# Kernel optimization log

Measured on AMD Instinct MI355X. Metric: run time of the kernel, lower is better.

Reference implementation:

```python
import jax, jax.numpy as jnp
import numpy as np

K_MASK = -2.3819763e+38

B, T, D = 2, 2048, 2048
N_HEADS, N_KV, HEAD_DIM = 16, 8, 128
SCALAR = 0.08838834764831845  # head_dim ** -0.5
ROPE_BASE = 10000


def rms_norm(x, scale):
    # fp32 mean-of-squares, rsqrt, bf16 round-trip, then scale (as in QwemmaRMSNorm)
    x32 = x.astype(jnp.float32)
    var = jnp.mean(jnp.square(x32), axis=-1, keepdims=True)
    rescaled = (x32 * jax.lax.rsqrt(var + 1e-06)).astype(jnp.bfloat16)
    return rescaled * scale


def apply_rope(inputs, positions, base_frequency):
    head_dim = inputs.shape[-1]
    fraction = 2 * jnp.arange(0, head_dim // 2) / head_dim
    timescale = base_frequency ** fraction
    sinusoid = positions[..., jnp.newaxis] / timescale[jnp.newaxis, jnp.newaxis, :]
    sinusoid = sinusoid[..., jnp.newaxis, :]  # [B,T,1,H/2]
    sin = jnp.sin(sinusoid).astype(inputs.dtype)
    cos = jnp.cos(sinusoid).astype(inputs.dtype)
    first, second = jnp.split(inputs, 2, axis=-1)
    out = jnp.concatenate([first * cos - second * sin,
                           second * cos + first * sin], axis=-1)
    return out.astype(inputs.dtype)


def setup_inputs() -> dict:
    key = jax.random.key(0)
    ks = jax.random.split(key, 7)
    x = jax.random.normal(ks[0], (B, T, D), dtype=jnp.float32)
    segment_pos = jnp.broadcast_to(jnp.arange(T, dtype=jnp.int32)[None, :], (B, T))
    attn_mask = jnp.broadcast_to(jnp.tril(jnp.ones((T, T), dtype=bool))[None], (B, T, T))
    q_w = jax.random.normal(ks[1], (N_HEADS, D, HEAD_DIM), dtype=jnp.float32) * 0.02
    kv_w = jax.random.normal(ks[2], (2, N_KV, D, HEAD_DIM), dtype=jnp.float32) * 0.02
    o_w = jax.random.normal(ks[3], (N_HEADS, HEAD_DIM, D), dtype=jnp.float32) * 0.02
    q_scale = 1.0 + 0.1 * jax.random.normal(ks[4], (HEAD_DIM,), dtype=jnp.float32)
    k_scale = 1.0 + 0.1 * jax.random.normal(ks[5], (HEAD_DIM,), dtype=jnp.float32)
    return {"x": x, "segment_pos": segment_pos, "attn_mask": attn_mask,
            "q_w": q_w, "kv_w": kv_w, "o_w": o_w,
            "q_scale": q_scale, "k_scale": k_scale}


def reference(x, segment_pos, attn_mask, q_w, kv_w, o_w, q_scale, k_scale):
    # projections
    q = jnp.einsum('BTD,NDH->BTNH', x, q_w)
    k, v = jnp.einsum('BSD,CKDH->CBSKH', x, kv_w)
    # QK RMSNorm + RoPE
    q = apply_rope(rms_norm(q, q_scale), segment_pos, ROPE_BASE)
    k = apply_rope(rms_norm(k, k_scale), segment_pos, ROPE_BASE)
    # GQA: [B,T,N,H] -> [B,T,K,G,H]
    b, t, n, h = q.shape
    g = n // N_KV
    q = q.reshape((b, t, N_KV, g, h))
    logits = jnp.einsum('BTKGH,BSKH->BTKGS', q, k)
    logits = (logits.astype(jnp.float32) * SCALAR).astype(jnp.bfloat16)
    s = logits.shape[-1]
    logits = logits.reshape((b, t, n, s))
    padded = jnp.where(jnp.expand_dims(attn_mask, -2), logits, K_MASK)
    probs = jax.nn.softmax(padded.astype(jnp.float32), axis=-1).astype(k.dtype)
    probs = probs.reshape((b, t, N_KV, g, s))
    encoded = jnp.einsum('BTKGS,BSKH->BTKGH', probs, v)
    encoded = encoded.reshape((b, t, n, h))
    return jnp.einsum('BTNH,NHD->BTD', encoded, o_w)


if __name__ == '__main__':
    out = reference(**setup_inputs())
    print(out.shape, out.dtype)
```

## Files before the change

### kernel.cpp

```cpp
#include <hip/hip_runtime.h>

typedef unsigned short u16;
typedef __attribute__((ext_vector_type(4))) float f32x4;
typedef __attribute__((ext_vector_type(8))) short s16x8;

#define SCALAR_F 0.08838834764831845f
#define KMASKF (-1e30f)

__device__ __forceinline__ u16 f2b(float f){
  unsigned u = __float_as_uint(f);
  unsigned r = u + 0x7FFFu + ((u>>16)&1u);
  return (u16)(r>>16);
}
__device__ __forceinline__ float b2f(u16 h){ return __uint_as_float(((unsigned)h)<<16); }

__device__ __forceinline__ f32x4 mfma16(s16x8 a, s16x8 b, f32x4 c){
  return __builtin_amdgcn_mfma_f32_16x16x32_bf16(a, b, c, 0, 0, 0);
}

__device__ __forceinline__ void glds16(const u16* g, u16* l){
  __builtin_amdgcn_global_load_lds((const __attribute__((address_space(1))) unsigned*)g,
                                   (__attribute__((address_space(3))) unsigned*)l, 16, 0, 0);
}

__global__ __launch_bounds__(256) void cvt_f32_bf16(const float* __restrict__ in, u16* __restrict__ out){
  int i = blockIdx.x*256 + threadIdx.x;
  const float4* p = (const float4*)in;
  float4 a = p[2*i], b = p[2*i+1];
  s16x8 r;
  r[0]=(short)f2b(a.x); r[1]=(short)f2b(a.y); r[2]=(short)f2b(a.z); r[3]=(short)f2b(a.w);
  r[4]=(short)f2b(b.x); r[5]=(short)f2b(b.y); r[6]=(short)f2b(b.z); r[7]=(short)f2b(b.w);
  *(s16x8*)(out + (size_t)i*8) = r;
}

__global__ __launch_bounds__(256) void build_wqkvt(const float* __restrict__ qw, const float* __restrict__ kvw,
                                                   u16* __restrict__ out){
  __shared__ float t[64][65];
  int head = blockIdx.z;
  int d0 = blockIdx.y*64, h0 = blockIdx.x*64;
  const float* src; int colbase;
  if (head < 16){ src = qw + (size_t)head*2048*128; colbase = head*128; }
  else if (head < 24){ int k = head-16; src = kvw + (size_t)k*2048*128; colbase = 2048 + k*128; }
  else { int k = head-24; src = kvw + (size_t)(8+k)*2048*128; colbase = 3072 + k*128; }
  int tid = threadIdx.x;
  #pragma unroll
  for (int p=0;p<16;p++){ int e = p*256+tid; int r = e>>6, c = e&63;
    t[r][c] = src[(size_t)(d0+r)*128 + h0 + c]; }
  __syncthreads();
  #pragma unroll
  for (int p=0;p<16;p++){ int e = p*256+tid; int c = e>>6, r = e&63;
    out[(size_t)(colbase + h0 + c)*2048 + d0 + r] = f2b(t[r][c]); }
}

__global__ __launch_bounds__(256) void tr2048(const float* __restrict__ src, u16* __restrict__ out){
  __shared__ float t[64][65];
  int r0 = blockIdx.y*64, c0 = blockIdx.x*64;
  int tid = threadIdx.x;
  #pragma unroll
  for (int p=0;p<16;p++){ int e = p*256+tid; int r = e>>6, c = e&63;
    t[r][c] = src[(size_t)(r0+r)*2048 + c0 + c]; }
  __syncthreads();
  #pragma unroll
  for (int p=0;p<16;p++){ int e = p*256+tid; int c = e>>6, r = e&63;
    out[(size_t)(c0+c)*2048 + r0 + r] = f2b(t[r][c]); }
}

__global__ __launch_bounds__(256) void rope_table(float* __restrict__ table){
  int tid = blockIdx.x*256 + threadIdx.x;
  int pos = tid>>6, i = tid&63;
  float ts = powf(10000.f, (float)i * (1.f/64.f));
  float ang = (float)pos / ts;
  ((float2*)table)[tid] = make_float2(sinf(ang), cosf(ang));
}

__global__ __launch_bounds__(512,2) void gemm256(const u16* __restrict__ A, const u16* __restrict__ Bt,
                                                 u16* __restrict__ C, int K, int ldc){
  __shared__ u16 Asw[4][256*32];
  __shared__ u16 Bsw[4][256*32];
  const int tid = threadIdx.x;
  const int wid = tid>>6, l = tid&63;
  const int wr = wid>>2, wc = wid&3;
  const int l15 = l&15, lg = l>>4;
  const int wg = blockIdx.x;
  const int swz = (wg&7)*32 + (wg>>3);
  const size_t m0 = (size_t)(swz>>4)*256, n0 = (size_t)(swz&15)*256;

  const f32x4 z4 = {0.f,0.f,0.f,0.f};
  f32x4 acc[8][4];
  #pragma unroll
  for (int mi=0;mi<8;mi++)
    #pragma unroll
    for (int ni=0;ni<4;ni++) acc[mi][ni] = z4;

  auto stage = [&](int k0, int bi){
    #pragma unroll
    for (int c=0;c<2;c++){
      int g = c*512 + tid;
      int row = g>>2;
      int sc = (g&3) ^ ((g>>3)&3);
      glds16(A  + (m0+row)*K + k0 + sc*8, &Asw[bi][0] + g*8);
      glds16(Bt + (n0+row)*K + k0 + sc*8, &Bsw[bi][0] + g*8);
    }
  };

  auto compute = [&](int bi){
    const char* AsB = (const char*)&Asw[bi][0];
    const char* BsB = (const char*)&Bsw[bi][0];
    s16x8 bfr[4];
    #pragma unroll
    for (int ni=0;ni<4;ni++){
      int r = wc*64 + ni*16 + l15;
      bfr[ni] = *(const s16x8*)(BsB + r*64 + ((lg*16) ^ (((r>>1)&3)<<4)));
    }
    __builtin_amdgcn_s_setprio(1);
    #pragma unroll
    for (int mi=0;mi<8;mi++){
      int r = wr*128 + mi*16 + l15;
      s16x8 af = *(const s16x8*)(AsB + r*64 + ((lg*16) ^ (((r>>1)&3)<<4)));
      #pragma unroll
      for (int ni=0;ni<4;ni++)
        acc[mi][ni] = mfma16(af, bfr[ni], acc[mi][ni]);
    }
    __builtin_amdgcn_s_setprio(0);
  };

  const int NT = K>>5;
  stage(0,0); stage(32,1); stage(64,2);
  asm volatile("s_waitcnt vmcnt(8)" ::: "memory");
  __builtin_amdgcn_s_barrier();
  for (int t=0; t<NT; ++t){
    if (t+3 < NT) stage((t+3)<<5, (t+3)&3);
    compute(t&3);
    int rem = NT-1-t;
    if (rem >= 3)      { asm volatile("s_waitcnt vmcnt(8)" ::: "memory"); }
    else if (rem == 2) { asm volatile("s_waitcnt vmcnt(4)" ::: "memory"); }
    else if (rem == 1) { asm volatile("s_waitcnt vmcnt(0)" ::: "memory"); }
    __builtin_amdgcn_s_barrier();
  }

  #pragma unroll
  for (int mi=0;mi<8;mi++)
    #pragma unroll
    for (int ni=0;ni<4;ni++)
      #pragma unroll
      for (int r=0;r<4;r++){
        size_t row = m0 + wr*128 + mi*16 + lg*4 + r;
        size_t col = n0 + wc*64 + ni*16 + l15;
        C[row*ldc + col] = f2b(acc[mi][ni][r]);
      }
}

template<bool OUTBF16>
__global__ __launch_bounds__(256) void gemm_bt(const u16* __restrict__ A, const u16* __restrict__ Bt,
                                               void* __restrict__ C, int K, int ldc){
  __shared__ u16 As[128*64];
  __shared__ u16 Bs[128*64];
  const int tid = threadIdx.x, w = tid>>6, l = tid&63;
  const int wm = w>>1, wn = w&1;
  const int l15 = l&15, lg = l>>4, l7 = l&7;
  const size_t m0 = (size_t)blockIdx.y*128, n0 = (size_t)blockIdx.x*128;
  const f32x4 z4 = {0.f,0.f,0.f,0.f};
  f32x4 acc[4][4];
  #pragma unroll
  for (int m=0;m<4;m++)
    #pragma unroll
    for (int n=0;n<4;n++) acc[m][n] = z4;
  const char* AsB = (const char*)As; const char* BsB = (const char*)Bs;
  int colsw[2];
  colsw[0] = (lg*16) ^ (l7<<4);
  colsw[1] = (64 + lg*16) ^ (l7<<4);
  int arow[4], brow[4];
  #pragma unroll
  for (int m=0;m<4;m++){ arow[m] = (wm*64 + m*16 + l15)*128; brow[m] = (wn*64 + m*16 + l15)*128; }
  const int sgl = l7 ^ (l>>3);
  for (int k0=0;k0<K;k0+=64){
    #pragma unroll
    for (int i=0;i<4;i++){
      int slot = (w*4+i)*64 + l;
      int row = slot>>3;
      glds16(A  + (m0+row)*K + k0 + sgl*8, (u16*)As + slot*8);
      glds16(Bt + (n0+row)*K + k0 + sgl*8, (u16*)Bs + slot*8);
    }
    __syncthreads();
    #pragma unroll
    for (int kb=0;kb<2;kb++){
      s16x8 af[4], bf[4];
      #pragma unroll
      for (int m=0;m<4;m++) af[m] = *(const s16x8*)(AsB + arow[m] + colsw[kb]);
      #pragma unroll
      for (int n=0;n<4;n++) bf[n] = *(const s16x8*)(BsB + brow[n] + colsw[kb]);
      #pragma unroll
      for (int m=0;m<4;m++)
        #pragma unroll
        for (int n=0;n<4;n++)
          acc[m][n] = mfma16(af[m], bf[n], acc[m][n]);
    }
    __syncthreads();
  }
  #pragma unroll
  for (int m=0;m<4;m++)
    #pragma unroll
    for (int n=0;n<4;n++)
      #pragma unroll
      for (int r=0;r<4;r++){
        size_t row = m0 + wm*64 + m*16 + lg*4 + r;
        size_t col = n0 + wn*64 + n*16 + l15;
        if (OUTBF16) ((u16*)C)[row*ldc + col] = f2b(acc[m][n][r]);
        else ((float*)C)[row*ldc + col] = acc[m][n][r];
      }
}

__global__ __launch_bounds__(256) void norm_rope(const u16* __restrict__ qkv, const float* __restrict__ table,
                                                 const float* __restrict__ scale, const int* __restrict__ segpos,
                                                 u16* __restrict__ dst, int nhl2, int colbase, float mult){
  int w = threadIdx.x>>6, l = threadIdx.x&63;
  int rid = blockIdx.x*4 + w;
  int bt = rid >> nhl2;
  int n  = rid & ((1<<nhl2)-1);
  int b = bt >> 11, t = bt & 2047;
  const u16* src = qkv + (size_t)bt*4096 + colbase + n*128;
  float x1 = b2f(src[l]), x2 = b2f(src[64+l]);
  float ss = x1*x1 + x2*x2;
  #pragma unroll
  for (int off=32; off; off>>=1) ss += __shfl_xor(ss, off);
  float rs = rsqrtf(ss*(1.f/128.f) + 1e-6f);
  float v1 = x1*rs*scale[l], v2 = x2*rs*scale[64+l];
  int pos = segpos[bt];
  float2 sc = ((const float2*)table)[pos*64 + l];
  float o1 = (v1*sc.y - v2*sc.x)*mult;
  float o2 = (v2*sc.y + v1*sc.x)*mult;
  u16* d = dst + (((size_t)((b<<nhl2) + n))*2048 + t)*128;
  d[l] = f2b(o1); d[64+l] = f2b(o2);
}

__global__ __launch_bounds__(256) void vtr(const u16* __restrict__ qkv, u16* __restrict__ vt){
  __shared__ float t[64][65];
  int bk = blockIdx.z;
  int t0 = blockIdx.y*64, d0 = blockIdx.x*64;
  int b = bk>>3, kv = bk&7;
  int tid = threadIdx.x;
  #pragma unroll
  for (int p=0;p<16;p++){ int e = p*256+tid; int r = e>>6, c = e&63;
    t[r][c] = b2f(qkv[(size_t)(b*2048 + t0 + r)*4096 + 3072 + kv*128 + d0 + c]); }
  __syncthreads();
  #pragma unroll
  for (int p=0;p<16;p++){ int e = p*256+tid; int c = e>>6, r = e&63;
    vt[((size_t)bk*128 + d0 + c)*2048 + t0 + r] = f2b(t[r][c]); }
}

__global__ __launch_bounds__(256,2) void attn_kern(const u16* __restrict__ qn, const u16* __restrict__ kn,
                                                   const u16* __restrict__ vt, u16* __restrict__ enc){
  __shared__ u16 Ks[2][64*128];
  __shared__ u16 Vs[2][64*128];
  __shared__ u16 Ps[4*16*64];
  const int idx = blockIdx.x;
  const int pp = idx>>5;
  const int hb = idx & 31;
  const int hn = hb & 15, b = hb >> 4;
  const int kv = hn>>1;
  const int tid = threadIdx.x, w = tid>>6, l = tid&63;
  const int l15 = l&15, lg = l>>4;
  const u16* qh = qn + ((size_t)(b*16+hn))*2048*128;
  const u16* kh = kn + ((size_t)(b*8+kv))*2048*128;
  const u16* vh = vt + ((size_t)(b*8+kv))*128*2048;
  const int qbA = pp, qbB = 31-pp;

  int qr0 = qbA*64 + w*16;
  s16x8 qf[4];
  #pragma unroll
  for (int kb=0;kb<4;kb++)
    qf[kb] = *(const s16x8*)(qh + (size_t)(qr0 + l15)*128 + kb*32 + lg*8);

  const f32x4 z4 = {0.f,0.f,0.f,0.f};
  f32x4 o[8];
  #pragma unroll
  for (int dn=0;dn<8;dn++) o[dn] = z4;
  float mrow[4], lp[4];
  #pragma unroll
  for (int r=0;r<4;r++){ mrow[r] = KMASKF; lp[r] = 0.f; }

  const char* KsB0 = (const char*)&Ks[0][0];
  const char* VsB0 = (const char*)&Vs[0][0];
  char* PsB = (char*)Ps + w*2048;

  auto stage = [&](int s0, int bi){
    #pragma unroll
    for (int i=0;i<4;i++){
      int slot = (w*4+i)*64 + l;
      { int row = slot>>4, g = slot&15, gl = g ^ (row&7);
        glds16(kh + (size_t)(s0+row)*128 + gl*8, &Ks[bi][0] + slot*8); }
      { int row = slot>>3, g = slot&7, gl = g ^ (row&7);
        glds16(vh + (size_t)row*2048 + s0 + gl*8, &Vs[bi][0] + slot*8); }
    }
  };

  auto epilogue = [&](int qr){
    #pragma unroll
    for (int r=0;r<4;r++){
      float s = lp[r];
      s += __shfl_xor(s,1); s += __shfl_xor(s,2); s += __shfl_xor(s,4); s += __shfl_xor(s,8);
      lp[r] = 1.f/s;
    }
    #pragma unroll
    for (int dn=0;dn<8;dn++)
      #pragma unroll
      for (int r=0;r<4;r++){
        size_t row = (size_t)b*2048 + qr + lg*4 + r;
        size_t col = hn*128 + dn*16 + l15;
        enc[row*2048 + col] = f2b(o[dn][r]*lp[r]);
      }
  };

  stage(0, 0);
  __syncthreads();

  int cur = 0;
  for (int it=0; it<=32; ++it){
    if (it < 32){
      int s0n = (it+1 <= pp) ? (it+1)*64 : (it-pp)*64;
      stage(s0n, cur^1);
    }
    const int s0 = (it <= pp) ? it*64 : (it-pp-1)*64;
    const char* KsB = KsB0 + cur*16384;
    const char* VsB = VsB0 + cur*16384;

    f32x4 sa[4];
    #pragma unroll
    for (int nc=0;nc<4;nc++) sa[nc] = z4;
    #pragma unroll
    for (int kb=0;kb<4;kb++){
      s16x8 kf[4];
      #pragma unroll
      for (int nc=0;nc<4;nc++){
        int srow = nc*16 + l15;
        int cb = (kb*64 + lg*16) ^ ((srow&7)<<4);
        kf[nc] = *(const s16x8*)(KsB + srow*256 + cb);
      }
      #pragma unroll
      for (int nc=0;nc<4;nc++)
        sa[nc] = mfma16(qf[kb], kf[nc], sa[nc]);
    }
    if (it == pp || it == 32){
      #pragma unroll
      for (int nc=0;nc<4;nc++)
        #pragma unroll
        for (int r=0;r<4;r++){
          int row = qr0 + lg*4 + r;
          int col = s0 + nc*16 + l15;
          if (col > row) sa[nc][r] = KMASKF;
        }
    }
    #pragma unroll
    for (int r=0;r<4;r++){
      float pm = fmaxf(fmaxf(sa[0][r], sa[1][r]), fmaxf(sa[2][r], sa[3][r]));
      pm = fmaxf(pm, __shfl_xor(pm,1));
      pm = fmaxf(pm, __shfl_xor(pm,2));
      pm = fmaxf(pm, __shfl_xor(pm,4));
      pm = fmaxf(pm, __shfl_xor(pm,8));
      float mo = mrow[r];
      float mn = fmaxf(mo, pm);
      float sc = __expf(mo - mn);
      mrow[r] = mn;
      int rowp = lg*4 + r;
      float ls = 0.f;
      #pragma unroll
      for (int nc=0;nc<4;nc++){
        float p = __expf(sa[nc][r] - mn);
        ls += p;
        int cb = ((nc*16 + l15)*2) ^ ((rowp&7)<<4);
        *(u16*)(PsB + rowp*128 + cb) = f2b(p);
      }
      lp[r] = lp[r]*sc + ls;
      #pragma unroll
      for (int dn=0;dn<8;dn++) o[dn][r] *= sc;
    }
    asm volatile("" ::: "memory");
    #pragma unroll
    for (int kb=0;kb<2;kb++){
      int rowp = l15;
      int cbp = (kb*64 + lg*16) ^ ((rowp&7)<<4);
      s16x8 pf = *(const s16x8*)(PsB + rowp*128 + cbp);
      #pragma unroll
      for (int dn=0;dn<8;dn++){
        int vrow = dn*16 + l15;
        int cb = (kb*64 + lg*16) ^ ((vrow&7)<<4);
        s16x8 vf = *(const s16x8*)(VsB + vrow*128 + cb);
        o[dn] = mfma16(pf, vf, o[dn]);
      }
    }
    if (it == pp){
      epilogue(qr0);
      qr0 = qbB*64 + w*16;
      #pragma unroll
      for (int kb=0;kb<4;kb++)
        qf[kb] = *(const s16x8*)(qh + (size_t)(qr0 + l15)*128 + kb*32 + lg*8);
      #pragma unroll
      for (int dn=0;dn<8;dn++) o[dn] = z4;
      #pragma unroll
      for (int r=0;r<4;r++){ mrow[r] = KMASKF; lp[r] = 0.f; }
    }
    __syncthreads();
    cur ^= 1;
  }
  epilogue(qr0);
}

extern "C" void kernel_launch(void* const* d_in, const int* in_sizes, int n_in,
                              void* d_out, int out_size, void* d_ws, size_t ws_size,
                              hipStream_t stream){
  const float* x      = (const float*)d_in[0];
  const int*   segpos = (const int*)d_in[1];
  const float* qw     = (const float*)d_in[3];
  const float* kvw    = (const float*)d_in[4];
  const float* ow     = (const float*)d_in[5];
  const float* qs     = (const float*)d_in[6];
  const float* ks     = (const float*)d_in[7];
  float* out = (float*)d_out;

  char* ws = (char*)d_ws;
  size_t off = 0;
  auto alloc = [&](size_t bytes)->void*{ void* p = ws + off; off += (bytes + 255) & ~(size_t)255; return p; };
  u16*   xb    = (u16*)alloc((size_t)4096*2048*2);
  u16*   wqkvt = (u16*)alloc((size_t)4096*2048*2);
  u16*   wot   = (u16*)alloc((size_t)2048*2048*2);
  u16*   qkv   = (u16*)alloc((size_t)4096*4096*2);
  u16*   qn    = (u16*)alloc((size_t)2*16*2048*128*2);
  u16*   kn    = (u16*)alloc((size_t)2*8*2048*128*2);
  u16*   vt    = (u16*)alloc((size_t)2*8*128*2048*2);
  u16*   enc   = (u16*)alloc((size_t)4096*2048*2);
  float* table = (float*)alloc((size_t)2048*64*2*4);

  cvt_f32_bf16<<<4096,256,0,stream>>>(x, xb);
  build_wqkvt<<<dim3(2,32,32),256,0,stream>>>(qw, kvw, wqkvt);
  tr2048<<<dim3(32,32),256,0,stream>>>(ow, wot);
  rope_table<<<512,256,0,stream>>>(table);
  gemm256<<<256,512,0,stream>>>(xb, wqkvt, qkv, 2048, 4096);
  norm_rope<<<16384,256,0,stream>>>(qkv, table, qs, segpos, qn, 4, 0,    SCALAR_F);
  norm_rope<<<8192, 256,0,stream>>>(qkv, table, ks, segpos, kn, 3, 2048, 1.0f);
  vtr<<<dim3(2,32,16),256,0,stream>>>(qkv, vt);
  attn_kern<<<512,256,0,stream>>>(qn, kn, vt, enc);
  gemm_bt<false><<<dim3(16,32),256,0,stream>>>(enc, wot, out, 2048, 2048);
}
```

Baseline: 380.6 us.

## Restructure gemm256 into an 8-wave ping-pong schedule with K=64 double-buffered tiles

Replaces the 4-stage, K=32 LDS ring buffer in the 256x256 GEMM with a double buffer of K=64 tiles, split into 128-row halves. Each iteration now runs four phases separated by barriers, and each phase interleaves LDS fragment reads, async global-to-LDS staging of the next B/A halves, and MFMA blocks. It also switches to an 8-way XOR swizzle on 128-byte rows. The aim is to overlap memory traffic with matrix-core work more tightly and to halve the loop trip count. In exchange it adds many more barriers, more register fragments, and delicate vmcnt bookkeeping that could stall or race.

```diff
diff --git a/kernel.cpp b/kernel.cpp
--- a/kernel.cpp
+++ b/kernel.cpp
@@ -22,6 +22,9 @@
   __builtin_amdgcn_global_load_lds((const __attribute__((address_space(1))) unsigned*)g,
                                    (__attribute__((address_space(3))) unsigned*)l, 16, 0, 0);
 }
+
+#define PHASE_BAR() asm volatile("s_barrier" ::: "memory")
+#define LGKM0()     do { asm volatile("s_waitcnt lgkmcnt(0)" ::: "memory"); __builtin_amdgcn_sched_barrier(0); } while(0)
 
 __global__ __launch_bounds__(256) void cvt_f32_bf16(const float* __restrict__ in, u16* __restrict__ out){
   int i = blockIdx.x*256 + threadIdx.x;
@@ -75,8 +78,8 @@
 
 __global__ __launch_bounds__(512,2) void gemm256(const u16* __restrict__ A, const u16* __restrict__ Bt,
                                                  u16* __restrict__ C, int K, int ldc){
-  __shared__ u16 Asw[4][256*32];
-  __shared__ u16 Bsw[4][256*32];
+  __shared__ u16 Als[2][2][128*64];
+  __shared__ u16 Bls[2][2][128*64];
   const int tid = threadIdx.x;
   const int wid = tid>>6, l = tid&63;
   const int wr = wid>>2, wc = wid&3;
@@ -92,50 +95,117 @@
     #pragma unroll
     for (int ni=0;ni<4;ni++) acc[mi][ni] = z4;
 
-  auto stage = [&](int k0, int bi){
+  auto stageA = [&](int k0, int bi, int h){
     #pragma unroll
     for (int c=0;c<2;c++){
       int g = c*512 + tid;
-      int row = g>>2;
-      int sc = (g&3) ^ ((g>>3)&3);
-      glds16(A  + (m0+row)*K + k0 + sc*8, &Asw[bi][0] + g*8);
-      glds16(Bt + (n0+row)*K + k0 + sc*8, &Bsw[bi][0] + g*8);
+      int row = g>>3, pg = g&7;
+      glds16(A + (m0 + h*128 + row)*K + k0 + ((pg ^ (row&7))<<3), &Als[bi][h][0] + g*8);
     }
   };
-
-  auto compute = [&](int bi){
-    const char* AsB = (const char*)&Asw[bi][0];
-    const char* BsB = (const char*)&Bsw[bi][0];
-    s16x8 bfr[4];
-    #pragma unroll
-    for (int ni=0;ni<4;ni++){
-      int r = wc*64 + ni*16 + l15;
-      bfr[ni] = *(const s16x8*)(BsB + r*64 + ((lg*16) ^ (((r>>1)&3)<<4)));
-    }
+  auto stageB = [&](int k0, int bi, int h){
+    #pragma unroll
+    for (int c=0;c<2;c++){
+      int g = c*512 + tid;
+      int row = g>>3, pg = g&7;
+      glds16(Bt + (n0 + h*128 + row)*K + k0 + ((pg ^ (row&7))<<3), &Bls[bi][h][0] + g*8);
+    }
+  };
+
+  s16x8 af[8][2], bf[4][2];
+
+  const int NT = K>>6;
+  stageA(0,0,0); stageA(0,0,1); stageB(0,0,0); stageB(0,0,1);
+  stageA(64,1,0); stageA(64,1,1);
+  asm volatile("s_waitcnt vmcnt(4)" ::: "memory");
+  PHASE_BAR();
+
+  for (int t=0; t<NT; ++t){
+    const int bi = t&1;
+    const char* Ab = (const char*)&Als[bi][wr][0];
+    const char* Bb = (const char*)&Bls[bi][wc>>1][0];
+    const int brl = (wc&1)*64;
+    const int kn1 = (t+1)<<6, kn2 = (t+2)<<6;
+
+    #pragma unroll
+    for (int mi=0;mi<4;mi++){
+      int r = mi*16 + l15;
+      #pragma unroll
+      for (int kk=0;kk<2;kk++)
+        af[mi][kk] = *(const s16x8*)(Ab + r*128 + (((kk*4+lg) ^ (r&7))<<4));
+    }
+    #pragma unroll
+    for (int ni=0;ni<2;ni++){
+      int r = brl + ni*16 + l15;
+      #pragma unroll
+      for (int kk=0;kk<2;kk++)
+        bf[ni][kk] = *(const s16x8*)(Bb + r*128 + (((kk*4+lg) ^ (r&7))<<4));
+    }
+    if (t+1 < NT) stageB(kn1, bi^1, 0);
+    PHASE_BAR(); LGKM0();
     __builtin_amdgcn_s_setprio(1);
     #pragma unroll
-    for (int mi=0;mi<8;mi++){
-      int r = wr*128 + mi*16 + l15;
-      s16x8 af = *(const s16x8*)(AsB + r*64 + ((lg*16) ^ (((r>>1)&3)<<4)));
-      #pragma unroll
-      for (int ni=0;ni<4;ni++)
-        acc[mi][ni] = mfma16(af, bfr[ni], acc[mi][ni]);
-    }
+    for (int mi=0;mi<4;mi++)
+      #pragma unroll
+      for (int ni=0;ni<2;ni++)
+        #pragma unroll
+        for (int kk=0;kk<2;kk++)
+          acc[mi][ni] = mfma16(af[mi][kk], bf[ni][kk], acc[mi][ni]);
     __builtin_amdgcn_s_setprio(0);
-  };
-
-  const int NT = K>>5;
-  stage(0,0); stage(32,1); stage(64,2);
-  asm volatile("s_waitcnt vmcnt(8)" ::: "memory");
-  __builtin_amdgcn_s_barrier();
-  for (int t=0; t<NT; ++t){
-    if (t+3 < NT) stage((t+3)<<5, (t+3)&3);
-    compute(t&3);
-    int rem = NT-1-t;
-    if (rem >= 3)      { asm volatile("s_waitcnt vmcnt(8)" ::: "memory"); }
-    else if (rem == 2) { asm volatile("s_waitcnt vmcnt(4)" ::: "memory"); }
-    else if (rem == 1) { asm volatile("s_waitcnt vmcnt(0)" ::: "memory"); }
-    __builtin_amdgcn_s_barrier();
+    PHASE_BAR();
+
+    #pragma unroll
+    for (int ni=2;ni<4;ni++){
+      int r = brl + ni*16 + l15;
+      #pragma unroll
+      for (int kk=0;kk<2;kk++)
+        bf[ni][kk] = *(const s16x8*)(Bb + r*128 + (((kk*4+lg) ^ (r&7))<<4));
+    }
+    if (t+1 < NT) stageB(kn1, bi^1, 1);
+    PHASE_BAR(); LGKM0();
+    __builtin_amdgcn_s_setprio(1);
+    #pragma unroll
+    for (int mi=0;mi<4;mi++)
+      #pragma unroll
+      for (int ni=2;ni<4;ni++)
+        #pragma unroll
+        for (int kk=0;kk<2;kk++)
+          acc[mi][ni] = mfma16(af[mi][kk], bf[ni][kk], acc[mi][ni]);
+    __builtin_amdgcn_s_setprio(0);
+    PHASE_BAR();
+
+    #pragma unroll
+    for (int mi=4;mi<8;mi++){
+      int r = mi*16 + l15;
+      #pragma unroll
+      for (int kk=0;kk<2;kk++)
+        af[mi][kk] = *(const s16x8*)(Ab + r*128 + (((kk*4+lg) ^ (r&7))<<4));
+    }
+    PHASE_BAR(); LGKM0();
+    __builtin_amdgcn_s_setprio(1);
+    #pragma unroll
+    for (int mi=4;mi<8;mi++)
+      #pragma unroll
+      for (int ni=2;ni<4;ni++)
+        #pragma unroll
+        for (int kk=0;kk<2;kk++)
+          acc[mi][ni] = mfma16(af[mi][kk], bf[ni][kk], acc[mi][ni]);
+    __builtin_amdgcn_s_setprio(0);
+    PHASE_BAR();
+
+    if (t+2 < NT){ stageA(kn2, bi, 0); stageA(kn2, bi, 1); }
+    __builtin_amdgcn_s_setprio(1);
+    #pragma unroll
+    for (int mi=4;mi<8;mi++)
+      #pragma unroll
+      for (int ni=0;ni<2;ni++)
+        #pragma unroll
+        for (int kk=0;kk<2;kk++)
+          acc[mi][ni] = mfma16(af[mi][kk], bf[ni][kk], acc[mi][ni]);
+    __builtin_amdgcn_s_setprio(0);
+    if (t < NT-2)      { asm volatile("s_waitcnt vmcnt(4)" ::: "memory"); }
+    else if (t == NT-2){ asm volatile("s_waitcnt vmcnt(0)" ::: "memory"); }
+    PHASE_BAR();
   }
 
   #pragma unroll
```

Result: faster. 358.6 us (-5.8%).
